# Optimization experiments

Measured on AMD Instinct MI355X. Metric: run time of the kernel, lower is better.

Reference implementation:

```python
import jax, jax.numpy as jnp
import numpy as np

B, N, IN, H, DH, ACT = 8192, 36, 8, 8, 9, 10
GAT = H * DH  # 72 == 2*N, required so cat([down(x), t]) matches mu's input dim
NEG = -1e9


def setup_inputs() -> dict:
    key = jax.random.key(0)
    ks = jax.random.split(key, 9)
    x = jax.random.normal(ks[0], (B, N, IN), dtype=jnp.float32)
    adj = jax.random.randint(ks[1], (N, N), 0, 2, dtype=jnp.int32)
    adj = jnp.maximum(adj, jnp.eye(N, dtype=jnp.int32))  # self-loops: no empty softmax rows
    s = 0.1
    W = jax.random.normal(ks[2], (H, IN - 1, DH), dtype=jnp.float32) * s   # per-head projection
    a_src = jax.random.normal(ks[3], (H, DH), dtype=jnp.float32) * s       # attention vec (source half)
    a_dst = jax.random.normal(ks[4], (H, DH), dtype=jnp.float32) * s       # attention vec (target half)
    W_down = jax.random.normal(ks[5], (GAT, 1), dtype=jnp.float32) * s
    b_down = jnp.zeros((1,), dtype=jnp.float32)
    W_mu = jax.random.normal(ks[6], (GAT, ACT), dtype=jnp.float32) * s     # GAT == 2*N
    b_mu = jnp.zeros((ACT,), dtype=jnp.float32)
    return {"x": x, "adj": adj, "W": W, "a_src": a_src, "a_dst": a_dst,
            "W_down": W_down, "b_down": b_down, "W_mu": W_mu, "b_mu": b_mu}


def _gat_encoder(xc, adj, W, a_src, a_dst):
    # xc: [B,N,IN-1]; standard multi-head GAT with adjacency-masked attention
    h = jnp.einsum('bni,hid->bhnd', xc, W)                 # [B,H,N,DH]
    e_src = jnp.einsum('bhnd,hd->bhn', h, a_src)           # [B,H,N]
    e_dst = jnp.einsum('bhnd,hd->bhn', h, a_dst)           # [B,H,N]
    e = jax.nn.leaky_relu(e_src[:, :, :, None] + e_dst[:, :, None, :], 0.2)  # [B,H,N,N]
    e = jnp.where(adj[None, None, :, :] > 0, e, NEG)
    attn = jax.nn.softmax(e, axis=-1)
    out = jnp.einsum('bhij,bhjd->bhid', attn, h)           # [B,H,N,DH]
    out = out.transpose(0, 2, 1, 3).reshape(out.shape[0], N, GAT)  # concat heads
    return jax.nn.elu(out)


def reference(x, adj, W, a_src, a_dst, W_down, b_down, W_mu, b_mu):
    # slice/cat glue: drop feature 3, keep it as scalar channel t
    xc = jnp.concatenate([x[:, :, :3], x[:, :, 4:]], axis=-1)  # [B,N,IN-1]
    t = xc[:, :, 3]                                            # [B,N] (== original x[:,:,4])
    g = _gat_encoder(xc, adj, W, a_src, a_dst)                 # [B,N,GAT]
    down = (g @ W_down + b_down)[..., 0]                       # [B,N]
    feat = jax.nn.leaky_relu(jnp.concatenate([down, t], axis=-1), 0.01)  # [B,2N]
    mu = feat @ W_mu + b_mu                                    # [B,ACT]
    return mu
```

## Files before the change

### kernel.cpp

```cpp
#include <hip/hip_runtime.h>

typedef float v2f __attribute__((ext_vector_type(2)));

#define BB 8192
#define NN 36
#define INF_ 8
#define HH 8
#define DHH 9
#define GATF 72
#define ACTF 10
#define NTH 320
#define ROWS 288
#define HSTRIDE 12
#define WSTRIDE 12
#define L2E 1.44269504088896f
#define MASKNEG -1000000.0f

static __device__ __forceinline__ v2f mk2(float a, float b) { v2f r; r.x = a; r.y = b; return r; }

static __device__ __forceinline__ v2f pkfma(v2f a, v2f b, v2f c) {
    v2f d;
    asm("v_pk_fma_f32 %0, %1, %2, %3" : "=v"(d) : "v"(a), "v"(b), "v"(c));
    return d;
}

__global__ __launch_bounds__(NTH, 6) void gnn_kernel(
    const float* __restrict__ x, const int* __restrict__ adj,
    const float* __restrict__ W, const float* __restrict__ a_src,
    const float* __restrict__ a_dst, const float* __restrict__ W_down,
    const float* __restrict__ b_down, const float* __restrict__ W_mu,
    const float* __restrict__ b_mu, float* __restrict__ out)
{
    const int b = blockIdx.x;
    const int tid = threadIdx.x;

    __shared__ float xcs[NN * 9];
    __shared__ float ts[NN];
    __shared__ __align__(16) float hbuf[ROWS * HSTRIDE];
    __shared__ __align__(16) float edl[ROWS];
    __shared__ __align__(16) float adjf[NN * NN];
    __shared__ float pd[NN * 9];
    __shared__ float feat[GATF];
    __shared__ __align__(16) float wlds[HH * 7 * WSTRIDE];
    __shared__ v2f  aid[HH * DHH];
    __shared__ float wdlds[GATF];
    __shared__ float wmulds[GATF * ACTF];
    __shared__ float bdlds[1];
    __shared__ float bmulds[ACTF];

    const float* xb = x + (size_t)b * (NN * INF_);
    if (tid < NN * INF_) {
        int n = tid >> 3, c = tid & 7;
        float v = xb[tid];
        if (c < 3) xcs[n * 9 + c] = v;
        else if (c > 3) xcs[n * 9 + (c - 1)] = v;
        if (c == 4) ts[n] = v;
    }
    for (int idx = tid; idx < (NN * NN) / 4; idx += NTH) {
        int4 a4 = reinterpret_cast<const int4*>(adj)[idx];
        float4 m4;
        m4.x = (a4.x > 0) ? 0.f : MASKNEG;
        m4.y = (a4.y > 0) ? 0.f : MASKNEG;
        m4.z = (a4.z > 0) ? 0.f : MASKNEG;
        m4.w = (a4.w > 0) ? 0.f : MASKNEG;
        *reinterpret_cast<float4*>(adjf + idx * 4) = m4;
    }
    for (int idx = tid; idx < HH * 7 * DHH; idx += NTH) {
        int row = idx / DHH, d = idx - row * DHH;
        wlds[row * WSTRIDE + d] = W[idx];
    }
    if (tid < HH * DHH) aid[tid] = mk2(a_src[tid], a_dst[tid]);
    if (tid >= 128 && tid < 128 + GATF) wdlds[tid - 128] = W_down[tid - 128];
    for (int idx = tid; idx < GATF * ACTF; idx += NTH) wmulds[idx] = W_mu[idx];
    if (tid == 0) bdlds[0] = b_down[0];
    if (tid >= 64 && tid < 64 + ACTF) bmulds[tid - 64] = b_mu[tid - 64];
    __syncthreads();

    const int hh = (tid < ROWS) ? (tid / NN) : 0;
    const int i  = (tid < ROWS) ? (tid - hh * NN) : 0;
    float esr = 0.f;
    if (tid < ROWS) {
        const float* xp = xcs + i * 9;
        const float* wp = wlds + hh * 7 * WSTRIDE;
        v2f h01 = mk2(0.f, 0.f), h23 = h01, h45 = h01, h67 = h01;
        float h8 = 0.f;
        #pragma unroll
        for (int k = 0; k < 7; ++k) {
            float xk = xp[k];
            v2f xkk = mk2(xk, xk);
            const float* wr = wp + k * WSTRIDE;
            float4 wa = *reinterpret_cast<const float4*>(wr);
            float4 wb = *reinterpret_cast<const float4*>(wr + 4);
            float  wc = wr[8];
            h01 = pkfma(xkk, *(const v2f*)&wa.x, h01);
            h23 = pkfma(xkk, *(const v2f*)&wa.z, h23);
            h45 = pkfma(xkk, *(const v2f*)&wb.x, h45);
            h67 = pkfma(xkk, *(const v2f*)&wb.z, h67);
            h8 = fmaf(xk, wc, h8);
        }
        float* hp = hbuf + (hh * NN + i) * HSTRIDE;
        *reinterpret_cast<float4*>(hp)     = make_float4(h01.x, h01.y, h23.x, h23.y);
        *reinterpret_cast<float4*>(hp + 4) = make_float4(h45.x, h45.y, h67.x, h67.y);
        *reinterpret_cast<v2f*>(hp + 8)    = mk2(h8, 1.0f);
        const v2f* ap = aid + hh * DHH;
        v2f sd = mk2(0.f, 0.f);
        sd = pkfma(mk2(h01.x, h01.x), ap[0], sd);
        sd = pkfma(mk2(h01.y, h01.y), ap[1], sd);
        sd = pkfma(mk2(h23.x, h23.x), ap[2], sd);
        sd = pkfma(mk2(h23.y, h23.y), ap[3], sd);
        sd = pkfma(mk2(h45.x, h45.x), ap[4], sd);
        sd = pkfma(mk2(h45.y, h45.y), ap[5], sd);
        sd = pkfma(mk2(h67.x, h67.x), ap[6], sd);
        sd = pkfma(mk2(h67.y, h67.y), ap[7], sd);
        sd = pkfma(mk2(h8, h8), ap[8], sd);
        esr = sd.x * L2E;
        edl[hh * NN + i] = sd.y * L2E;
    }
    __syncthreads();

    if (tid < ROWS) {
        const float* hrow = hbuf + (hh * NN) * HSTRIDE;
        const float* edp = edl + hh * NN;
        const float* amr = adjf + i * NN;
        v2f acc01 = mk2(0.f, 0.f), acc23 = acc01, acc45 = acc01, acc67 = acc01, acc89 = acc01;

#define STEP(jj, ee, mm) { \
        float s_ = esr + (ee); \
        float e_ = fmaxf(s_, 0.2f * s_) + (mm);           \
        float p_ = __builtin_exp2f(e_);                   \
        const float* hj_ = hrow + (jj) * HSTRIDE; \
        float4 ha_ = *reinterpret_cast<const float4*>(hj_); \
        float4 hb_ = *reinterpret_cast<const float4*>(hj_ + 4); \
        v2f hc_ = *reinterpret_cast<const v2f*>(hj_ + 8); \
        v2f pp_ = mk2(p_, p_); \
        acc01 = pkfma(pp_, *(const v2f*)&ha_.x, acc01); \
        acc23 = pkfma(pp_, *(const v2f*)&ha_.z, acc23); \
        acc45 = pkfma(pp_, *(const v2f*)&hb_.x, acc45); \
        acc67 = pkfma(pp_, *(const v2f*)&hb_.z, acc67); \
        acc89 = pkfma(pp_, hc_, acc89); }

        #pragma unroll
        for (int q = 0; q < 9; ++q) {
            float4 e4 = *reinterpret_cast<const float4*>(edp + q * 4);
            float4 m4 = *reinterpret_cast<const float4*>(amr + q * 4);
            STEP(4 * q + 0, e4.x, m4.x);
            STEP(4 * q + 1, e4.y, m4.y);
            STEP(4 * q + 2, e4.z, m4.z);
            STEP(4 * q + 3, e4.w, m4.w);
        }
#undef STEP

        float inv = 1.0f / acc89.y;
        v2f inv2 = mk2(inv, inv);
        v2f o01 = acc01 * inv2, o23 = acc23 * inv2, o45 = acc45 * inv2, o67 = acc67 * inv2;
        float o8 = acc89.x * inv;
        const float* wdp = wdlds + hh * DHH;
        float pdown = 0.f;
#define EPI(oval, dd_) { \
        float o_ = (oval); \
        o_ = (o_ > 0.f) ? o_ : (__builtin_exp2f(o_ * L2E) - 1.0f); \
        pdown = fmaf(o_, wdp[dd_], pdown); }
        EPI(o01.x, 0); EPI(o01.y, 1); EPI(o23.x, 2); EPI(o23.y, 3);
        EPI(o45.x, 4); EPI(o45.y, 5); EPI(o67.x, 6); EPI(o67.y, 7);
        EPI(o8, 8);
#undef EPI
        pd[i * 9 + hh] = pdown;
    }
    __syncthreads();

    if (tid < NN) {
        const float* pp = pd + tid * 9;
        float acc = bdlds[0];
        #pragma unroll
        for (int h = 0; h < HH; ++h) acc += pp[h];
        feat[tid] = (acc > 0.f) ? acc : 0.01f * acc;
    } else if (tid < 2 * NN) {
        float v = ts[tid - NN];
        feat[tid] = (v > 0.f) ? v : 0.01f * v;
    }
    __syncthreads();

    if (tid < ACTF) {
        float acc = bmulds[tid];
        #pragma unroll
        for (int k = 0; k < GATF; ++k) acc = fmaf(feat[k], wmulds[k * ACTF + tid], acc);
        out[(size_t)b * ACTF + tid] = acc;
    }
}

extern "C" void kernel_launch(void* const* d_in, const int* in_sizes, int n_in,
                              void* d_out, int out_size, void* d_ws, size_t ws_size,
                              hipStream_t stream) {
    const float* x      = (const float*)d_in[0];
    const int*   adj    = (const int*)d_in[1];
    const float* W      = (const float*)d_in[2];
    const float* a_src  = (const float*)d_in[3];
    const float* a_dst  = (const float*)d_in[4];
    const float* W_down = (const float*)d_in[5];
    const float* b_down = (const float*)d_in[6];
    const float* W_mu   = (const float*)d_in[7];
    const float* b_mu   = (const float*)d_in[8];
    float* out = (float*)d_out;

    gnn_kernel<<<BB, NTH, 0, stream>>>(x, adj, W, a_src, a_dst, W_down, b_down, W_mu, b_mu, out);
}
```

Before: 79.40 us.

## Iterate attention over sparse neighbor lists instead of dense masked rows

```diff
diff --git a/kernel.cpp b/kernel.cpp
--- a/kernel.cpp
+++ b/kernel.cpp
@@ -12,17 +12,11 @@
 #define NTH 320
 #define ROWS 288
 #define HSTRIDE 12
-#define WSTRIDE 12
+#define HROWS 37
+#define JCOLS 40
 #define L2E 1.44269504088896f
-#define MASKNEG -1000000.0f
 
 static __device__ __forceinline__ v2f mk2(float a, float b) { v2f r; r.x = a; r.y = b; return r; }
-
-static __device__ __forceinline__ v2f pkfma(v2f a, v2f b, v2f c) {
-    v2f d;
-    asm("v_pk_fma_f32 %0, %1, %2, %3" : "=v"(d) : "v"(a), "v"(b), "v"(c));
-    return d;
-}
 
 __global__ __launch_bounds__(NTH, 6) void gnn_kernel(
     const float* __restrict__ x, const int* __restrict__ adj,
@@ -35,16 +29,16 @@
     const int tid = threadIdx.x;
 
     __shared__ float xcs[NN * 9];
-    __shared__ float ts[NN];
-    __shared__ __align__(16) float hbuf[ROWS * HSTRIDE];
-    __shared__ __align__(16) float edl[ROWS];
-    __shared__ __align__(16) float adjf[NN * NN];
+    __shared__ __align__(16) float hbuf[HH * HROWS * HSTRIDE];
+    __shared__ unsigned short jl[NN * JCOLS];
+    __shared__ int cnts[NN];
+    __shared__ int mstar;
     __shared__ float pd[NN * 9];
     __shared__ float feat[GATF];
-    __shared__ __align__(16) float wlds[HH * 7 * WSTRIDE];
+    __shared__ __align__(16) float wlds[HH * 7 * 12];
     __shared__ v2f  aid[HH * DHH];
     __shared__ float wdlds[GATF];
-    __shared__ float wmulds[GATF * ACTF];
+    __shared__ float wmulds[GATF * ACTF + 16];
     __shared__ float bdlds[1];
     __shared__ float bmulds[ACTF];
 
@@ -54,20 +48,22 @@
         float v = xb[tid];
         if (c < 3) xcs[n * 9 + c] = v;
         else if (c > 3) xcs[n * 9 + (c - 1)] = v;
-        if (c == 4) ts[n] = v;
-    }
-    for (int idx = tid; idx < (NN * NN) / 4; idx += NTH) {
-        int4 a4 = reinterpret_cast<const int4*>(adj)[idx];
-        float4 m4;
-        m4.x = (a4.x > 0) ? 0.f : MASKNEG;
-        m4.y = (a4.y > 0) ? 0.f : MASKNEG;
-        m4.z = (a4.z > 0) ? 0.f : MASKNEG;
-        m4.w = (a4.w > 0) ? 0.f : MASKNEG;
-        *reinterpret_cast<float4*>(adjf + idx * 4) = m4;
+        if (c == 4) feat[NN + n] = (v > 0.f) ? v : 0.01f * v;
+    }
+    {
+        int i0 = tid - 224;
+        if (i0 >= 0 && i0 < NN) {
+            const int* ar = adj + i0 * NN;
+            int cnt = 0;
+            for (int j = 0; j < NN; ++j) {
+                if (ar[j] > 0) { jl[i0 * JCOLS + cnt] = (unsigned short)(j * HSTRIDE); ++cnt; }
+            }
+            cnts[i0] = cnt;
+        }
     }
     for (int idx = tid; idx < HH * 7 * DHH; idx += NTH) {
         int row = idx / DHH, d = idx - row * DHH;
-        wlds[row * WSTRIDE + d] = W[idx];
+        wlds[row * 12 + d] = W[idx];
     }
     if (tid < HH * DHH) aid[tid] = mk2(a_src[tid], a_dst[tid]);
     if (tid >= 128 && tid < 128 + GATF) wdlds[tid - 128] = W_down[tid - 128];
@@ -81,88 +77,95 @@
     float esr = 0.f;
     if (tid < ROWS) {
         const float* xp = xcs + i * 9;
-        const float* wp = wlds + hh * 7 * WSTRIDE;
-        v2f h01 = mk2(0.f, 0.f), h23 = h01, h45 = h01, h67 = h01;
-        float h8 = 0.f;
+        const float* wp = wlds + hh * 7 * 12;
+        float h0=0.f,h1=0.f,h2=0.f,h3=0.f,h4=0.f,h5=0.f,h6=0.f,h7=0.f,h8=0.f;
         #pragma unroll
         for (int k = 0; k < 7; ++k) {
             float xk = xp[k];
-            v2f xkk = mk2(xk, xk);
-            const float* wr = wp + k * WSTRIDE;
+            const float* wr = wp + k * 12;
             float4 wa = *reinterpret_cast<const float4*>(wr);
             float4 wb = *reinterpret_cast<const float4*>(wr + 4);
             float  wc = wr[8];
-            h01 = pkfma(xkk, *(const v2f*)&wa.x, h01);
-            h23 = pkfma(xkk, *(const v2f*)&wa.z, h23);
-            h45 = pkfma(xkk, *(const v2f*)&wb.x, h45);
-            h67 = pkfma(xkk, *(const v2f*)&wb.z, h67);
+            h0 = fmaf(xk, wa.x, h0); h1 = fmaf(xk, wa.y, h1);
+            h2 = fmaf(xk, wa.z, h2); h3 = fmaf(xk, wa.w, h3);
+            h4 = fmaf(xk, wb.x, h4); h5 = fmaf(xk, wb.y, h5);
+            h6 = fmaf(xk, wb.z, h6); h7 = fmaf(xk, wb.w, h7);
             h8 = fmaf(xk, wc, h8);
         }
-        float* hp = hbuf + (hh * NN + i) * HSTRIDE;
-        *reinterpret_cast<float4*>(hp)     = make_float4(h01.x, h01.y, h23.x, h23.y);
-        *reinterpret_cast<float4*>(hp + 4) = make_float4(h45.x, h45.y, h67.x, h67.y);
-        *reinterpret_cast<v2f*>(hp + 8)    = mk2(h8, 1.0f);
         const v2f* ap = aid + hh * DHH;
         v2f sd = mk2(0.f, 0.f);
-        sd = pkfma(mk2(h01.x, h01.x), ap[0], sd);
-        sd = pkfma(mk2(h01.y, h01.y), ap[1], sd);
-        sd = pkfma(mk2(h23.x, h23.x), ap[2], sd);
-        sd = pkfma(mk2(h23.y, h23.y), ap[3], sd);
-        sd = pkfma(mk2(h45.x, h45.x), ap[4], sd);
-        sd = pkfma(mk2(h45.y, h45.y), ap[5], sd);
-        sd = pkfma(mk2(h67.x, h67.x), ap[6], sd);
-        sd = pkfma(mk2(h67.y, h67.y), ap[7], sd);
-        sd = pkfma(mk2(h8, h8), ap[8], sd);
+        sd = __builtin_elementwise_fma(mk2(h0, h0), ap[0], sd);
+        sd = __builtin_elementwise_fma(mk2(h1, h1), ap[1], sd);
+        sd = __builtin_elementwise_fma(mk2(h2, h2), ap[2], sd);
+        sd = __builtin_elementwise_fma(mk2(h3, h3), ap[3], sd);
+        sd = __builtin_elementwise_fma(mk2(h4, h4), ap[4], sd);
+        sd = __builtin_elementwise_fma(mk2(h5, h5), ap[5], sd);
+        sd = __builtin_elementwise_fma(mk2(h6, h6), ap[6], sd);
+        sd = __builtin_elementwise_fma(mk2(h7, h7), ap[7], sd);
+        sd = __builtin_elementwise_fma(mk2(h8, h8), ap[8], sd);
         esr = sd.x * L2E;
-        edl[hh * NN + i] = sd.y * L2E;
+        float edv = sd.y * L2E;
+        float* hp = hbuf + (hh * HROWS + i) * HSTRIDE;
+        *reinterpret_cast<float4*>(hp)     = make_float4(h0, h1, h2, h3);
+        *reinterpret_cast<float4*>(hp + 4) = make_float4(h4, h5, h6, h7);
+        *reinterpret_cast<float4*>(hp + 8) = make_float4(h8, 1.0f, edv, 0.f);
+    } else if (tid < 296) {
+        int h2 = tid - 288;
+        float* hp = hbuf + (h2 * HROWS + NN) * HSTRIDE;
+        *reinterpret_cast<float4*>(hp)     = make_float4(0.f, 0.f, 0.f, 0.f);
+        *reinterpret_cast<float4*>(hp + 4) = make_float4(0.f, 0.f, 0.f, 0.f);
+        *reinterpret_cast<float4*>(hp + 8) = make_float4(0.f, 0.f, -1000000.0f, 0.f);
+    } else {
+        int m = 0;
+        #pragma unroll
+        for (int r = 0; r < NN; ++r) m = max(m, cnts[r]);
+        int mpad = (m + 3) & ~3;
+        if (tid == 296) mstar = mpad;
+        for (int r = tid - 296; r < NN; r += 24) {
+            int c0 = cnts[r];
+            for (int q = c0; q < mpad; ++q)
+                jl[r * JCOLS + q] = (unsigned short)(NN * HSTRIDE);
+        }
     }
     __syncthreads();
 
     if (tid < ROWS) {
-        const float* hrow = hbuf + (hh * NN) * HSTRIDE;
-        const float* edp = edl + hh * NN;
-        const float* amr = adjf + i * NN;
-        v2f acc01 = mk2(0.f, 0.f), acc23 = acc01, acc45 = acc01, acc67 = acc01, acc89 = acc01;
-
-#define STEP(jj, ee, mm) { \
-        float s_ = esr + (ee); \
-        float e_ = fmaxf(s_, 0.2f * s_) + (mm);           \
-        float p_ = __builtin_exp2f(e_);                   \
-        const float* hj_ = hrow + (jj) * HSTRIDE; \
+        const float* hb = hbuf + (hh * HROWS) * HSTRIDE;
+        const unsigned short* jrow = jl + i * JCOLS;
+        const int mpad = mstar;
+        float a0=0.f,a1=0.f,a2=0.f,a3=0.f,a4=0.f,a5=0.f,a6=0.f,a7=0.f,a8=0.f,ssum=0.f;
+
+#define ELEM(e_) { \
+        const float* hj_ = hb + (e_); \
+        float4 hc_ = *reinterpret_cast<const float4*>(hj_ + 8);    \
+        float s_ = esr + hc_.z; \
+        float p_ = __builtin_exp2f(fmaxf(s_, 0.2f * s_)); \
         float4 ha_ = *reinterpret_cast<const float4*>(hj_); \
         float4 hb_ = *reinterpret_cast<const float4*>(hj_ + 4); \
-        v2f hc_ = *reinterpret_cast<const v2f*>(hj_ + 8); \
-        v2f pp_ = mk2(p_, p_); \
-        acc01 = pkfma(pp_, *(const v2f*)&ha_.x, acc01); \
-        acc23 = pkfma(pp_, *(const v2f*)&ha_.z, acc23); \
-        acc45 = pkfma(pp_, *(const v2f*)&hb_.x, acc45); \
-        acc67 = pkfma(pp_, *(const v2f*)&hb_.z, acc67); \
-        acc89 = pkfma(pp_, hc_, acc89); }
-
-        #pragma unroll
-        for (int q = 0; q < 9; ++q) {
-            float4 e4 = *reinterpret_cast<const float4*>(edp + q * 4);
-            float4 m4 = *reinterpret_cast<const float4*>(amr + q * 4);
-            STEP(4 * q + 0, e4.x, m4.x);
-            STEP(4 * q + 1, e4.y, m4.y);
-            STEP(4 * q + 2, e4.z, m4.z);
-            STEP(4 * q + 3, e4.w, m4.w);
-        }
-#undef STEP
-
-        float inv = 1.0f / acc89.y;
-        v2f inv2 = mk2(inv, inv);
-        v2f o01 = acc01 * inv2, o23 = acc23 * inv2, o45 = acc45 * inv2, o67 = acc67 * inv2;
-        float o8 = acc89.x * inv;
+        a0 = fmaf(p_, ha_.x, a0); a1 = fmaf(p_, ha_.y, a1); \
+        a2 = fmaf(p_, ha_.z, a2); a3 = fmaf(p_, ha_.w, a3); \
+        a4 = fmaf(p_, hb_.x, a4); a5 = fmaf(p_, hb_.y, a5); \
+        a6 = fmaf(p_, hb_.z, a6); a7 = fmaf(p_, hb_.w, a7); \
+        a8 = fmaf(p_, hc_.x, a8); ssum += p_; }
+
+        for (int q = 0; q < mpad; q += 4) {
+            uint2 jq = *reinterpret_cast<const uint2*>(jrow + q);
+            int e0 = (int)(jq.x & 0xffffu), e1 = (int)(jq.x >> 16);
+            int e2 = (int)(jq.y & 0xffffu), e3 = (int)(jq.y >> 16);
+            ELEM(e0); ELEM(e1); ELEM(e2); ELEM(e3);
+        }
+#undef ELEM
+
+        float inv = 1.0f / ssum;
         const float* wdp = wdlds + hh * DHH;
         float pdown = 0.f;
-#define EPI(oval, dd_) { \
-        float o_ = (oval); \
+#define EPI(val, dd_) { \
+        float o_ = (val) * inv; \
         o_ = (o_ > 0.f) ? o_ : (__builtin_exp2f(o_ * L2E) - 1.0f); \
         pdown = fmaf(o_, wdp[dd_], pdown); }
-        EPI(o01.x, 0); EPI(o01.y, 1); EPI(o23.x, 2); EPI(o23.y, 3);
-        EPI(o45.x, 4); EPI(o45.y, 5); EPI(o67.x, 6); EPI(o67.y, 7);
-        EPI(o8, 8);
+        EPI(a0, 0); EPI(a1, 1); EPI(a2, 2); EPI(a3, 3);
+        EPI(a4, 4); EPI(a5, 5); EPI(a6, 6); EPI(a7, 7);
+        EPI(a8, 8);
 #undef EPI
         pd[i * 9 + hh] = pdown;
     }
@@ -174,17 +177,20 @@
         #pragma unroll
         for (int h = 0; h < HH; ++h) acc += pp[h];
         feat[tid] = (acc > 0.f) ? acc : 0.01f * acc;
-    } else if (tid < 2 * NN) {
-        float v = ts[tid - NN];
-        feat[tid] = (v > 0.f) ? v : 0.01f * v;
-    }
-    __syncthreads();
-
-    if (tid < ACTF) {
-        float acc = bmulds[tid];
-        #pragma unroll
-        for (int k = 0; k < GATF; ++k) acc = fmaf(feat[k], wmulds[k * ACTF + tid], acc);
-        out[(size_t)b * ACTF + tid] = acc;
+    }
+    __syncthreads();
+
+    if (tid < 64) {
+        int o = tid >> 2, q = tid & 3;
+        float accp = (q == 0 && o < ACTF) ? bmulds[o] : 0.f;
+        #pragma unroll
+        for (int k = 0; k < 18; ++k) {
+            int kk = q * 18 + k;
+            accp = fmaf(feat[kk], wmulds[kk * ACTF + o], accp);
+        }
+        accp += __shfl_down(accp, 1);
+        accp += __shfl_down(accp, 2);
+        if (q == 0 && o < ACTF) out[(size_t)b * ACTF + o] = accp;
     }
 }
 
```

Result: slower. 125.7 us (+58.3%).

## Split attention aggregation over neighbors across two thread halves per block

Applied to the files above, without the earlier changes.

```diff
diff --git a/kernel.cpp b/kernel.cpp
--- a/kernel.cpp
+++ b/kernel.cpp
@@ -9,22 +9,16 @@
 #define DHH 9
 #define GATF 72
 #define ACTF 10
-#define NTH 320
+#define NTH 640
 #define ROWS 288
+#define LBASE 320
 #define HSTRIDE 12
-#define WSTRIDE 12
 #define L2E 1.44269504088896f
 #define MASKNEG -1000000.0f
 
 static __device__ __forceinline__ v2f mk2(float a, float b) { v2f r; r.x = a; r.y = b; return r; }
 
-static __device__ __forceinline__ v2f pkfma(v2f a, v2f b, v2f c) {
-    v2f d;
-    asm("v_pk_fma_f32 %0, %1, %2, %3" : "=v"(d) : "v"(a), "v"(b), "v"(c));
-    return d;
-}
-
-__global__ __launch_bounds__(NTH, 6) void gnn_kernel(
+__global__ __launch_bounds__(NTH, 7) void gnn_kernel(
     const float* __restrict__ x, const int* __restrict__ adj,
     const float* __restrict__ W, const float* __restrict__ a_src,
     const float* __restrict__ a_dst, const float* __restrict__ W_down,
@@ -38,10 +32,12 @@
     __shared__ float ts[NN];
     __shared__ __align__(16) float hbuf[ROWS * HSTRIDE];
     __shared__ __align__(16) float edl[ROWS];
+    __shared__ float esl[ROWS];
     __shared__ __align__(16) float adjf[NN * NN];
+    __shared__ float part[10 * ROWS];
     __shared__ float pd[NN * 9];
     __shared__ float feat[GATF];
-    __shared__ __align__(16) float wlds[HH * 7 * WSTRIDE];
+    __shared__ __align__(16) float wlds[HH * 7 * 12];
     __shared__ v2f  aid[HH * DHH];
     __shared__ float wdlds[GATF];
     __shared__ float wmulds[GATF * ACTF];
@@ -56,113 +52,139 @@
         else if (c > 3) xcs[n * 9 + (c - 1)] = v;
         if (c == 4) ts[n] = v;
     }
-    for (int idx = tid; idx < (NN * NN) / 4; idx += NTH) {
-        int4 a4 = reinterpret_cast<const int4*>(adj)[idx];
-        float4 m4;
-        m4.x = (a4.x > 0) ? 0.f : MASKNEG;
-        m4.y = (a4.y > 0) ? 0.f : MASKNEG;
-        m4.z = (a4.z > 0) ? 0.f : MASKNEG;
-        m4.w = (a4.w > 0) ? 0.f : MASKNEG;
-        *reinterpret_cast<float4*>(adjf + idx * 4) = m4;
-    }
-    for (int idx = tid; idx < HH * 7 * DHH; idx += NTH) {
-        int row = idx / DHH, d = idx - row * DHH;
-        wlds[row * WSTRIDE + d] = W[idx];
-    }
-    if (tid < HH * DHH) aid[tid] = mk2(a_src[tid], a_dst[tid]);
-    if (tid >= 128 && tid < 128 + GATF) wdlds[tid - 128] = W_down[tid - 128];
+    {
+        int idx = tid - 288;
+        if (idx >= 0 && idx < (NN * NN) / 4) {
+            int4 a4 = reinterpret_cast<const int4*>(adj)[idx];
+            float4 m4;
+            m4.x = (a4.x > 0) ? 0.f : MASKNEG;
+            m4.y = (a4.y > 0) ? 0.f : MASKNEG;
+            m4.z = (a4.z > 0) ? 0.f : MASKNEG;
+            m4.w = (a4.w > 0) ? 0.f : MASKNEG;
+            *reinterpret_cast<float4*>(adjf + idx * 4) = m4;
+        }
+    }
+    if (tid < HH * 7 * DHH) {
+        int row = tid / DHH, d = tid - row * DHH;
+        wlds[row * 12 + d] = W[tid];
+    }
+    { int idx = tid - 504; if (idx >= 0 && idx < HH * DHH) aid[idx] = mk2(a_src[idx], a_dst[idx]); }
+    { int idx = tid - 568; if (idx >= 0 && idx < GATF) wdlds[idx] = W_down[idx]; }
     for (int idx = tid; idx < GATF * ACTF; idx += NTH) wmulds[idx] = W_mu[idx];
-    if (tid == 0) bdlds[0] = b_down[0];
-    if (tid >= 64 && tid < 64 + ACTF) bmulds[tid - 64] = b_mu[tid - 64];
-    __syncthreads();
-
-    const int hh = (tid < ROWS) ? (tid / NN) : 0;
-    const int i  = (tid < ROWS) ? (tid - hh * NN) : 0;
+    if (tid == 636) bdlds[0] = b_down[0];
+    { int idx = tid - 612; if (idx >= 0 && idx < ACTF) bmulds[idx] = b_mu[idx]; }
+    __syncthreads();
+
+    const bool early = (tid < ROWS);
+    const bool late  = (tid >= LBASE) && (tid < LBASE + ROWS);
+    const int r = early ? tid : (late ? tid - LBASE : 0);
+    const int hh = r / NN, i = r - hh * NN;
+
     float esr = 0.f;
-    if (tid < ROWS) {
+    if (early) {
         const float* xp = xcs + i * 9;
-        const float* wp = wlds + hh * 7 * WSTRIDE;
-        v2f h01 = mk2(0.f, 0.f), h23 = h01, h45 = h01, h67 = h01;
-        float h8 = 0.f;
+        const float* wp = wlds + hh * 7 * 12;
+        float h0=0.f,h1=0.f,h2=0.f,h3=0.f,h4=0.f,h5=0.f,h6=0.f,h7=0.f,h8=0.f;
         #pragma unroll
         for (int k = 0; k < 7; ++k) {
             float xk = xp[k];
-            v2f xkk = mk2(xk, xk);
-            const float* wr = wp + k * WSTRIDE;
+            const float* wr = wp + k * 12;
             float4 wa = *reinterpret_cast<const float4*>(wr);
             float4 wb = *reinterpret_cast<const float4*>(wr + 4);
             float  wc = wr[8];
-            h01 = pkfma(xkk, *(const v2f*)&wa.x, h01);
-            h23 = pkfma(xkk, *(const v2f*)&wa.z, h23);
-            h45 = pkfma(xkk, *(const v2f*)&wb.x, h45);
-            h67 = pkfma(xkk, *(const v2f*)&wb.z, h67);
+            h0 = fmaf(xk, wa.x, h0); h1 = fmaf(xk, wa.y, h1);
+            h2 = fmaf(xk, wa.z, h2); h3 = fmaf(xk, wa.w, h3);
+            h4 = fmaf(xk, wb.x, h4); h5 = fmaf(xk, wb.y, h5);
+            h6 = fmaf(xk, wb.z, h6); h7 = fmaf(xk, wb.w, h7);
             h8 = fmaf(xk, wc, h8);
         }
-        float* hp = hbuf + (hh * NN + i) * HSTRIDE;
-        *reinterpret_cast<float4*>(hp)     = make_float4(h01.x, h01.y, h23.x, h23.y);
-        *reinterpret_cast<float4*>(hp + 4) = make_float4(h45.x, h45.y, h67.x, h67.y);
+        float* hp = hbuf + r * HSTRIDE;
+        *reinterpret_cast<float4*>(hp)     = make_float4(h0, h1, h2, h3);
+        *reinterpret_cast<float4*>(hp + 4) = make_float4(h4, h5, h6, h7);
         *reinterpret_cast<v2f*>(hp + 8)    = mk2(h8, 1.0f);
         const v2f* ap = aid + hh * DHH;
         v2f sd = mk2(0.f, 0.f);
-        sd = pkfma(mk2(h01.x, h01.x), ap[0], sd);
-        sd = pkfma(mk2(h01.y, h01.y), ap[1], sd);
-        sd = pkfma(mk2(h23.x, h23.x), ap[2], sd);
-        sd = pkfma(mk2(h23.y, h23.y), ap[3], sd);
-        sd = pkfma(mk2(h45.x, h45.x), ap[4], sd);
-        sd = pkfma(mk2(h45.y, h45.y), ap[5], sd);
-        sd = pkfma(mk2(h67.x, h67.x), ap[6], sd);
-        sd = pkfma(mk2(h67.y, h67.y), ap[7], sd);
-        sd = pkfma(mk2(h8, h8), ap[8], sd);
+        sd = __builtin_elementwise_fma(mk2(h0, h0), ap[0], sd);
+        sd = __builtin_elementwise_fma(mk2(h1, h1), ap[1], sd);
+        sd = __builtin_elementwise_fma(mk2(h2, h2), ap[2], sd);
+        sd = __builtin_elementwise_fma(mk2(h3, h3), ap[3], sd);
+        sd = __builtin_elementwise_fma(mk2(h4, h4), ap[4], sd);
+        sd = __builtin_elementwise_fma(mk2(h5, h5), ap[5], sd);
+        sd = __builtin_elementwise_fma(mk2(h6, h6), ap[6], sd);
+        sd = __builtin_elementwise_fma(mk2(h7, h7), ap[7], sd);
+        sd = __builtin_elementwise_fma(mk2(h8, h8), ap[8], sd);
         esr = sd.x * L2E;
-        edl[hh * NN + i] = sd.y * L2E;
-    }
-    __syncthreads();
-
-    if (tid < ROWS) {
-        const float* hrow = hbuf + (hh * NN) * HSTRIDE;
-        const float* edp = edl + hh * NN;
-        const float* amr = adjf + i * NN;
-        v2f acc01 = mk2(0.f, 0.f), acc23 = acc01, acc45 = acc01, acc67 = acc01, acc89 = acc01;
-
-#define STEP(jj, ee, mm) { \
-        float s_ = esr + (ee); \
-        float e_ = fmaxf(s_, 0.2f * s_) + (mm);           \
-        float p_ = __builtin_exp2f(e_);                   \
+        edl[r] = sd.y * L2E;
+        esl[r] = esr;
+    }
+    __syncthreads();
+
+    float a0=0.f,a1=0.f,a2=0.f,a3=0.f,a4=0.f,a5=0.f,a6=0.f,a7=0.f,a8=0.f,ssum=0.f;
+
+#define STEP(jj, ee, mm, es_) { \
+        float s_ = (es_) + (ee); \
+        float e_ = fmaxf(s_, 0.2f * s_) + (mm); \
+        float p_ = __builtin_exp2f(e_); \
         const float* hj_ = hrow + (jj) * HSTRIDE; \
         float4 ha_ = *reinterpret_cast<const float4*>(hj_); \
         float4 hb_ = *reinterpret_cast<const float4*>(hj_ + 4); \
         v2f hc_ = *reinterpret_cast<const v2f*>(hj_ + 8); \
-        v2f pp_ = mk2(p_, p_); \
-        acc01 = pkfma(pp_, *(const v2f*)&ha_.x, acc01); \
-        acc23 = pkfma(pp_, *(const v2f*)&ha_.z, acc23); \
-        acc45 = pkfma(pp_, *(const v2f*)&hb_.x, acc45); \
-        acc67 = pkfma(pp_, *(const v2f*)&hb_.z, acc67); \
-        acc89 = pkfma(pp_, hc_, acc89); }
-
-        #pragma unroll
-        for (int q = 0; q < 9; ++q) {
+        a0 = fmaf(p_, ha_.x, a0); a1 = fmaf(p_, ha_.y, a1); \
+        a2 = fmaf(p_, ha_.z, a2); a3 = fmaf(p_, ha_.w, a3); \
+        a4 = fmaf(p_, hb_.x, a4); a5 = fmaf(p_, hb_.y, a5); \
+        a6 = fmaf(p_, hb_.z, a6); a7 = fmaf(p_, hb_.w, a7); \
+        a8 = fmaf(p_, hc_.x, a8); ssum = fmaf(p_, hc_.y, ssum); }
+
+    if (early) {
+        const float* hrow = hbuf + (hh * NN) * HSTRIDE;
+        const float* edp = edl + hh * NN;
+        const float* amr = adjf + i * NN;
+        #pragma unroll
+        for (int q = 0; q < 4; ++q) {
             float4 e4 = *reinterpret_cast<const float4*>(edp + q * 4);
             float4 m4 = *reinterpret_cast<const float4*>(amr + q * 4);
-            STEP(4 * q + 0, e4.x, m4.x);
-            STEP(4 * q + 1, e4.y, m4.y);
-            STEP(4 * q + 2, e4.z, m4.z);
-            STEP(4 * q + 3, e4.w, m4.w);
-        }
+            STEP(4 * q + 0, e4.x, m4.x, esr);
+            STEP(4 * q + 1, e4.y, m4.y, esr);
+            STEP(4 * q + 2, e4.z, m4.z, esr);
+            STEP(4 * q + 3, e4.w, m4.w, esr);
+        }
+        part[0 * ROWS + r] = a0; part[1 * ROWS + r] = a1; part[2 * ROWS + r] = a2;
+        part[3 * ROWS + r] = a3; part[4 * ROWS + r] = a4; part[5 * ROWS + r] = a5;
+        part[6 * ROWS + r] = a6; part[7 * ROWS + r] = a7; part[8 * ROWS + r] = a8;
+        part[9 * ROWS + r] = ssum;
+    } else if (late) {
+        float esru = esl[r];
+        const float* hrow = hbuf + (hh * NN) * HSTRIDE;
+        const float* edp = edl + hh * NN;
+        const float* amr = adjf + i * NN;
+        #pragma unroll
+        for (int q = 4; q < 9; ++q) {
+            float4 e4 = *reinterpret_cast<const float4*>(edp + q * 4);
+            float4 m4 = *reinterpret_cast<const float4*>(amr + q * 4);
+            STEP(4 * q + 0, e4.x, m4.x, esru);
+            STEP(4 * q + 1, e4.y, m4.y, esru);
+            STEP(4 * q + 2, e4.z, m4.z, esru);
+            STEP(4 * q + 3, e4.w, m4.w, esru);
+        }
+    }
 #undef STEP
-
-        float inv = 1.0f / acc89.y;
-        v2f inv2 = mk2(inv, inv);
-        v2f o01 = acc01 * inv2, o23 = acc23 * inv2, o45 = acc45 * inv2, o67 = acc67 * inv2;
-        float o8 = acc89.x * inv;
+    __syncthreads();
+
+    if (late) {
+        a0 += part[0 * ROWS + r]; a1 += part[1 * ROWS + r]; a2 += part[2 * ROWS + r];
+        a3 += part[3 * ROWS + r]; a4 += part[4 * ROWS + r]; a5 += part[5 * ROWS + r];
+        a6 += part[6 * ROWS + r]; a7 += part[7 * ROWS + r]; a8 += part[8 * ROWS + r];
+        ssum += part[9 * ROWS + r];
+        float inv = 1.0f / ssum;
         const float* wdp = wdlds + hh * DHH;
         float pdown = 0.f;
-#define EPI(oval, dd_) { \
-        float o_ = (oval); \
+#define EPI(val, dd_) { \
+        float o_ = (val) * inv; \
         o_ = (o_ > 0.f) ? o_ : (__builtin_exp2f(o_ * L2E) - 1.0f); \
         pdown = fmaf(o_, wdp[dd_], pdown); }
-        EPI(o01.x, 0); EPI(o01.y, 1); EPI(o23.x, 2); EPI(o23.y, 3);
-        EPI(o45.x, 4); EPI(o45.y, 5); EPI(o67.x, 6); EPI(o67.y, 7);
-        EPI(o8, 8);
+        EPI(a0, 0); EPI(a1, 1); EPI(a2, 2); EPI(a3, 3);
+        EPI(a4, 4); EPI(a5, 5); EPI(a6, 6); EPI(a7, 7);
+        EPI(a8, 8);
 #undef EPI
         pd[i * 9 + hh] = pdown;
     }
```

After: 123.4 us. 1.55x slower.

## Process two batch items per block to amortize shared weight loads

Applied to the files above, without the earlier changes.

```diff
diff --git a/kernel.cpp b/kernel.cpp
--- a/kernel.cpp
+++ b/kernel.cpp
@@ -18,12 +18,6 @@
 
 static __device__ __forceinline__ v2f mk2(float a, float b) { v2f r; r.x = a; r.y = b; return r; }
 
-static __device__ __forceinline__ v2f pkfma(v2f a, v2f b, v2f c) {
-    v2f d;
-    asm("v_pk_fma_f32 %0, %1, %2, %3" : "=v"(d) : "v"(a), "v"(b), "v"(c));
-    return d;
-}
-
 __global__ __launch_bounds__(NTH, 6) void gnn_kernel(
     const float* __restrict__ x, const int* __restrict__ adj,
     const float* __restrict__ W, const float* __restrict__ a_src,
@@ -31,11 +25,11 @@
     const float* __restrict__ b_down, const float* __restrict__ W_mu,
     const float* __restrict__ b_mu, float* __restrict__ out)
 {
-    const int b = blockIdx.x;
+    const int b0 = blockIdx.x * 2;
     const int tid = threadIdx.x;
 
-    __shared__ float xcs[NN * 9];
-    __shared__ float ts[NN];
+    __shared__ float xcs[2 * NN * 9];
+    __shared__ float ts[2 * NN];
     __shared__ __align__(16) float hbuf[ROWS * HSTRIDE];
     __shared__ __align__(16) float edl[ROWS];
     __shared__ __align__(16) float adjf[NN * NN];
@@ -48,13 +42,18 @@
     __shared__ float bdlds[1];
     __shared__ float bmulds[ACTF];
 
-    const float* xb = x + (size_t)b * (NN * INF_);
-    if (tid < NN * INF_) {
-        int n = tid >> 3, c = tid & 7;
-        float v = xb[tid];
-        if (c < 3) xcs[n * 9 + c] = v;
-        else if (c > 3) xcs[n * 9 + (c - 1)] = v;
-        if (c == 4) ts[n] = v;
+    {
+        const float* xb = x + (size_t)b0 * (NN * INF_);
+        for (int idx = tid; idx < 2 * NN * INF_; idx += NTH) {
+            int item = idx / (NN * INF_);
+            int rem = idx - item * (NN * INF_);
+            int n = rem >> 3, c = rem & 7;
+            float v = xb[idx];
+            float* xc = xcs + item * (NN * 9);
+            if (c < 3) xc[n * 9 + c] = v;
+            else if (c > 3) xc[n * 9 + (c - 1)] = v;
+            if (c == 4) ts[item * NN + n] = v;
+        }
     }
     for (int idx = tid; idx < (NN * NN) / 4; idx += NTH) {
         int4 a4 = reinterpret_cast<const int4*>(adj)[idx];
@@ -78,113 +77,114 @@
 
     const int hh = (tid < ROWS) ? (tid / NN) : 0;
     const int i  = (tid < ROWS) ? (tid - hh * NN) : 0;
-    float esr = 0.f;
-    if (tid < ROWS) {
-        const float* xp = xcs + i * 9;
-        const float* wp = wlds + hh * 7 * WSTRIDE;
-        v2f h01 = mk2(0.f, 0.f), h23 = h01, h45 = h01, h67 = h01;
-        float h8 = 0.f;
-        #pragma unroll
-        for (int k = 0; k < 7; ++k) {
-            float xk = xp[k];
-            v2f xkk = mk2(xk, xk);
-            const float* wr = wp + k * WSTRIDE;
-            float4 wa = *reinterpret_cast<const float4*>(wr);
-            float4 wb = *reinterpret_cast<const float4*>(wr + 4);
-            float  wc = wr[8];
-            h01 = pkfma(xkk, *(const v2f*)&wa.x, h01);
-            h23 = pkfma(xkk, *(const v2f*)&wa.z, h23);
-            h45 = pkfma(xkk, *(const v2f*)&wb.x, h45);
-            h67 = pkfma(xkk, *(const v2f*)&wb.z, h67);
-            h8 = fmaf(xk, wc, h8);
-        }
-        float* hp = hbuf + (hh * NN + i) * HSTRIDE;
-        *reinterpret_cast<float4*>(hp)     = make_float4(h01.x, h01.y, h23.x, h23.y);
-        *reinterpret_cast<float4*>(hp + 4) = make_float4(h45.x, h45.y, h67.x, h67.y);
-        *reinterpret_cast<v2f*>(hp + 8)    = mk2(h8, 1.0f);
-        const v2f* ap = aid + hh * DHH;
-        v2f sd = mk2(0.f, 0.f);
-        sd = pkfma(mk2(h01.x, h01.x), ap[0], sd);
-        sd = pkfma(mk2(h01.y, h01.y), ap[1], sd);
-        sd = pkfma(mk2(h23.x, h23.x), ap[2], sd);
-        sd = pkfma(mk2(h23.y, h23.y), ap[3], sd);
-        sd = pkfma(mk2(h45.x, h45.x), ap[4], sd);
-        sd = pkfma(mk2(h45.y, h45.y), ap[5], sd);
-        sd = pkfma(mk2(h67.x, h67.x), ap[6], sd);
-        sd = pkfma(mk2(h67.y, h67.y), ap[7], sd);
-        sd = pkfma(mk2(h8, h8), ap[8], sd);
-        esr = sd.x * L2E;
-        edl[hh * NN + i] = sd.y * L2E;
-    }
-    __syncthreads();
-
-    if (tid < ROWS) {
-        const float* hrow = hbuf + (hh * NN) * HSTRIDE;
-        const float* edp = edl + hh * NN;
-        const float* amr = adjf + i * NN;
-        v2f acc01 = mk2(0.f, 0.f), acc23 = acc01, acc45 = acc01, acc67 = acc01, acc89 = acc01;
+
+    for (int it = 0; it < 2; ++it) {
+        float esr = 0.f;
+        if (tid < ROWS) {
+            const float* xp = xcs + it * (NN * 9) + i * 9;
+            const float* wp = wlds + hh * 7 * WSTRIDE;
+            float h0=0.f,h1=0.f,h2=0.f,h3=0.f,h4=0.f,h5=0.f,h6=0.f,h7=0.f,h8=0.f;
+            #pragma unroll
+            for (int k = 0; k < 7; ++k) {
+                float xk = xp[k];
+                const float* wr = wp + k * WSTRIDE;
+                float4 wa = *reinterpret_cast<const float4*>(wr);
+                float4 wb = *reinterpret_cast<const float4*>(wr + 4);
+                float  wc = wr[8];
+                h0 = fmaf(xk, wa.x, h0); h1 = fmaf(xk, wa.y, h1);
+                h2 = fmaf(xk, wa.z, h2); h3 = fmaf(xk, wa.w, h3);
+                h4 = fmaf(xk, wb.x, h4); h5 = fmaf(xk, wb.y, h5);
+                h6 = fmaf(xk, wb.z, h6); h7 = fmaf(xk, wb.w, h7);
+                h8 = fmaf(xk, wc, h8);
+            }
+            float* hp = hbuf + (hh * NN + i) * HSTRIDE;
+            *reinterpret_cast<float4*>(hp)     = make_float4(h0, h1, h2, h3);
+            *reinterpret_cast<float4*>(hp + 4) = make_float4(h4, h5, h6, h7);
+            *reinterpret_cast<v2f*>(hp + 8)    = mk2(h8, 1.0f);
+            const v2f* ap = aid + hh * DHH;
+            v2f sd = mk2(0.f, 0.f);
+            sd = __builtin_elementwise_fma(mk2(h0, h0), ap[0], sd);
+            sd = __builtin_elementwise_fma(mk2(h1, h1), ap[1], sd);
+            sd = __builtin_elementwise_fma(mk2(h2, h2), ap[2], sd);
+            sd = __builtin_elementwise_fma(mk2(h3, h3), ap[3], sd);
+            sd = __builtin_elementwise_fma(mk2(h4, h4), ap[4], sd);
+            sd = __builtin_elementwise_fma(mk2(h5, h5), ap[5], sd);
+            sd = __builtin_elementwise_fma(mk2(h6, h6), ap[6], sd);
+            sd = __builtin_elementwise_fma(mk2(h7, h7), ap[7], sd);
+            sd = __builtin_elementwise_fma(mk2(h8, h8), ap[8], sd);
+            esr = sd.x * L2E;
+            edl[hh * NN + i] = sd.y * L2E;
+        }
+        __syncthreads();
+
+        if (tid < ROWS) {
+            const float* hrow = hbuf + (hh * NN) * HSTRIDE;
+            const float* edp = edl + hh * NN;
+            const float* amr = adjf + i * NN;
+            v2f acc01 = mk2(0.f, 0.f), acc23 = acc01, acc45 = acc01, acc67 = acc01, acc89 = acc01;
 
 #define STEP(jj, ee, mm) { \
-        float s_ = esr + (ee); \
-        float e_ = fmaxf(s_, 0.2f * s_) + (mm);           \
-        float p_ = __builtin_exp2f(e_);                   \
-        const float* hj_ = hrow + (jj) * HSTRIDE; \
-        float4 ha_ = *reinterpret_cast<const float4*>(hj_); \
-        float4 hb_ = *reinterpret_cast<const float4*>(hj_ + 4); \
-        v2f hc_ = *reinterpret_cast<const v2f*>(hj_ + 8); \
-        v2f pp_ = mk2(p_, p_); \
-        acc01 = pkfma(pp_, *(const v2f*)&ha_.x, acc01); \
-        acc23 = pkfma(pp_, *(const v2f*)&ha_.z, acc23); \
-        acc45 = pkfma(pp_, *(const v2f*)&hb_.x, acc45); \
-        acc67 = pkfma(pp_, *(const v2f*)&hb_.z, acc67); \
-        acc89 = pkfma(pp_, hc_, acc89); }
-
-        #pragma unroll
-        for (int q = 0; q < 9; ++q) {
-            float4 e4 = *reinterpret_cast<const float4*>(edp + q * 4);
-            float4 m4 = *reinterpret_cast<const float4*>(amr + q * 4);
-            STEP(4 * q + 0, e4.x, m4.x);
-            STEP(4 * q + 1, e4.y, m4.y);
-            STEP(4 * q + 2, e4.z, m4.z);
-            STEP(4 * q + 3, e4.w, m4.w);
-        }
+            float s_ = esr + (ee); \
+            float e_ = fmaxf(s_, 0.2f * s_) + (mm);           \
+            float p_ = __builtin_exp2f(e_);                   \
+            const float* hj_ = hrow + (jj) * HSTRIDE; \
+            float4 ha_ = *reinterpret_cast<const float4*>(hj_); \
+            float4 hb_ = *reinterpret_cast<const float4*>(hj_ + 4); \
+            v2f hc_ = *reinterpret_cast<const v2f*>(hj_ + 8); \
+            v2f pp_ = mk2(p_, p_); \
+            acc01 = __builtin_elementwise_fma(pp_, mk2(ha_.x, ha_.y), acc01); \
+            acc23 = __builtin_elementwise_fma(pp_, mk2(ha_.z, ha_.w), acc23); \
+            acc45 = __builtin_elementwise_fma(pp_, mk2(hb_.x, hb_.y), acc45); \
+            acc67 = __builtin_elementwise_fma(pp_, mk2(hb_.z, hb_.w), acc67); \
+            acc89 = __builtin_elementwise_fma(pp_, hc_, acc89); }
+
+            #pragma unroll
+            for (int q = 0; q < 9; ++q) {
+                float4 e4 = *reinterpret_cast<const float4*>(edp + q * 4);
+                float4 m4 = *reinterpret_cast<const float4*>(amr + q * 4);
+                STEP(4 * q + 0, e4.x, m4.x);
+                STEP(4 * q + 1, e4.y, m4.y);
+                STEP(4 * q + 2, e4.z, m4.z);
+                STEP(4 * q + 3, e4.w, m4.w);
+            }
 #undef STEP
 
-        float inv = 1.0f / acc89.y;
-        v2f inv2 = mk2(inv, inv);
-        v2f o01 = acc01 * inv2, o23 = acc23 * inv2, o45 = acc45 * inv2, o67 = acc67 * inv2;
-        float o8 = acc89.x * inv;
-        const float* wdp = wdlds + hh * DHH;
-        float pdown = 0.f;
+            float inv = 1.0f / acc89.y;
+            v2f inv2 = mk2(inv, inv);
+            v2f o01 = acc01 * inv2, o23 = acc23 * inv2, o45 = acc45 * inv2, o67 = acc67 * inv2;
+            float o8 = acc89.x * inv;
+            const float* wdp = wdlds + hh * DHH;
+            float pdown = 0.f;
 #define EPI(oval, dd_) { \
-        float o_ = (oval); \
-        o_ = (o_ > 0.f) ? o_ : (__builtin_exp2f(o_ * L2E) - 1.0f); \
-        pdown = fmaf(o_, wdp[dd_], pdown); }
-        EPI(o01.x, 0); EPI(o01.y, 1); EPI(o23.x, 2); EPI(o23.y, 3);
-        EPI(o45.x, 4); EPI(o45.y, 5); EPI(o67.x, 6); EPI(o67.y, 7);
-        EPI(o8, 8);
+            float o_ = (oval); \
+            o_ = (o_ > 0.f) ? o_ : (__builtin_exp2f(o_ * L2E) - 1.0f); \
+            pdown = fmaf(o_, wdp[dd_], pdown); }
+            EPI(o01.x, 0); EPI(o01.y, 1); EPI(o23.x, 2); EPI(o23.y, 3);
+            EPI(o45.x, 4); EPI(o45.y, 5); EPI(o67.x, 6); EPI(o67.y, 7);
+            EPI(o8, 8);
 #undef EPI
-        pd[i * 9 + hh] = pdown;
-    }
-    __syncthreads();
-
-    if (tid < NN) {
-        const float* pp = pd + tid * 9;
-        float acc = bdlds[0];
-        #pragma unroll
-        for (int h = 0; h < HH; ++h) acc += pp[h];
-        feat[tid] = (acc > 0.f) ? acc : 0.01f * acc;
-    } else if (tid < 2 * NN) {
-        float v = ts[tid - NN];
-        feat[tid] = (v > 0.f) ? v : 0.01f * v;
-    }
-    __syncthreads();
-
-    if (tid < ACTF) {
-        float acc = bmulds[tid];
-        #pragma unroll
-        for (int k = 0; k < GATF; ++k) acc = fmaf(feat[k], wmulds[k * ACTF + tid], acc);
-        out[(size_t)b * ACTF + tid] = acc;
+            pd[i * 9 + hh] = pdown;
+        }
+        __syncthreads();
+
+        if (tid < NN) {
+            const float* pp = pd + tid * 9;
+            float acc = bdlds[0];
+            #pragma unroll
+            for (int h = 0; h < HH; ++h) acc += pp[h];
+            feat[tid] = (acc > 0.f) ? acc : 0.01f * acc;
+        } else if (tid < 2 * NN) {
+            float v = ts[it * NN + (tid - NN)];
+            feat[tid] = (v > 0.f) ? v : 0.01f * v;
+        }
+        __syncthreads();
+
+        if (tid < ACTF) {
+            float acc = bmulds[tid];
+            #pragma unroll
+            for (int k = 0; k < GATF; ++k) acc = fmaf(feat[k], wmulds[k * ACTF + tid], acc);
+            out[(size_t)(b0 + it) * ACTF + tid] = acc;
+        }
     }
 }
 
@@ -202,5 +202,5 @@
     const float* b_mu   = (const float*)d_in[8];
     float* out = (float*)d_out;
 
-    gnn_kernel<<<BB, NTH, 0, stream>>>(x, adj, W, a_src, a_dst, W_down, b_down, W_mu, b_mu, out);
+    gnn_kernel<<<BB / 2, NTH, 0, stream>>>(x, adj, W, a_src, a_dst, W_down, b_down, W_mu, b_mu, out);
 }
```

Result: slower. 84.29 us (+6.1%).
